# Performance work log

Hardware: AMD Instinct MI355X
Metric: run time of the kernel (lower is better)

## Reference

```python
import jax, jax.numpy as jnp
import numpy as np
import math

NUM_HEADS = 2


def setup_inputs() -> dict:
    key = jax.random.key(0)
    k1, k2, k3, k4 = jax.random.split(key, 4)
    B, S, E = 16, 2048, 8  # embed_dim == n_wires == 8 (required by module structure)
    x = jax.random.normal(k1, (B, S, E), dtype=jnp.float32)
    theta = jax.random.normal(k2, (E,), dtype=jnp.float32)          # trainable RX angles, one per wire
    w_out = jax.random.normal(k3, (E, E), dtype=jnp.float32) / math.sqrt(E)  # out_proj weight
    b_out = jax.random.normal(k4, (E,), dtype=jnp.float32) * 0.01   # out_proj bias
    return {"x": x, "theta": theta, "w_out": w_out, "b_out": b_out}


def reference(x, theta, w_out, b_out):
    B, S, E = x.shape
    H = NUM_HEADS
    dk = E // H
    # Quantum projection, analytic form: per-wire RX(x) then RX(theta) on |0>,
    # PauliZ expectation -> cos(x + theta). Same layer applied for q, k, v.
    q = jnp.cos(x + theta)              # [B, S, E]
    qh = q.reshape(B, S, H, dk).transpose(0, 2, 1, 3)  # [B, H, S, dk]; q == k == v
    scores = jnp.einsum('bhqd,bhkd->bhqk', qh, qh) / jnp.sqrt(jnp.float32(dk))
    attn = jax.nn.softmax(scores, axis=-1)             # dropout is identity in eval
    out = jnp.einsum('bhqk,bhkd->bhqd', attn, qh)      # [B, H, S, dk]
    out = out.transpose(0, 2, 1, 3).reshape(B, S, E)
    return out @ w_out.T + b_out
```

## Files before the change

kernel.cpp:

```cpp
#include <hip/hip_runtime.h>
#include <math.h>

#define BB 16
#define SS 2048
#define EE 8
#define HH 2
#define ROWS 128
#define TILES (SS / ROWS)
#define NCHUNK 4
#define CHUNK (SS / NCHUNK)
#define THREADS 512

typedef float vf2 __attribute__((ext_vector_type(2)));

#if defined(__has_builtin)
#if __has_builtin(__builtin_elementwise_fma)
#define HAS_EW_FMA 1
#endif
#endif

__device__ __forceinline__ float fast_exp2(float x) {
#if defined(__has_builtin)
#if __has_builtin(__builtin_amdgcn_exp2f)
  return __builtin_amdgcn_exp2f(x);
#else
  return exp2f(x);
#endif
#else
  return exp2f(x);
#endif
}

__device__ __forceinline__ vf2 pk_fma(vf2 a, vf2 b, vf2 c) {
#ifdef HAS_EW_FMA
  return __builtin_elementwise_fma(a, b, c);
#else
  vf2 r; r.x = fmaf(a.x, b.x, c.x); r.y = fmaf(a.y, b.y, c.y); return r;
#endif
}

__global__ __launch_bounds__(THREADS, 4)
void qattn_kernel(const float* __restrict__ x,
                  const float* __restrict__ theta,
                  const float* __restrict__ w_out,
                  const float* __restrict__ b_out,
                  float* __restrict__ out) {
  __shared__ float4 kv[HH * SS];

  const int b    = blockIdx.x >> 4;
  const int tile = blockIdx.x & 15;
  const int t    = threadIdx.x;

  const float4 th0 = ((const float4*)theta)[0];
  const float4 th1 = ((const float4*)theta)[1];

  const float4* x4 = (const float4*)x + (size_t)b * (SS * 2);
  for (int idx = t; idx < SS * 2; idx += THREADS) {
    const int s  = idx >> 1;
    const int hf = idx & 1;
    float4 xr = x4[idx];
    float4 th = hf ? th1 : th0;
    float4 kvv;
    kvv.x = cosf(xr.x + th.x);
    kvv.y = cosf(xr.y + th.y);
    kvv.z = cosf(xr.z + th.z);
    kvv.w = cosf(xr.w + th.w);
    kv[hf * SS + s] = kvv;
  }
  __syncthreads();

  const int lane = t & 63;
  const int w    = t >> 6;
  const int h    = w & 1;
  const int jc   = w >> 1;
  const int r0   = tile * ROWS + lane;
  const int r1   = r0 + 64;

  const float K_SCALE = 0.72134752044448170367f;
  float4 q0 = kv[h * SS + r0];
  float4 q1 = kv[h * SS + r1];
  vf2 q0xy = {q0.x * K_SCALE, q0.y * K_SCALE};
  vf2 q0zw = {q0.z * K_SCALE, q0.w * K_SCALE};
  vf2 q1xy = {q1.x * K_SCALE, q1.y * K_SCALE};
  vf2 q1zw = {q1.z * K_SCALE, q1.w * K_SCALE};

  float l0 = 0.f, l1 = 0.f;
  vf2 a0xy = {0.f, 0.f}, a0zw = {0.f, 0.f};
  vf2 a1xy = {0.f, 0.f}, a1zw = {0.f, 0.f};
  const float4* kp = &kv[h * SS + jc * CHUNK];
#pragma unroll 4
  for (int j = 0; j < CHUNK; ++j) {
    float4 k4 = kp[j];
    vf2 kxy = {k4.x, k4.y};
    vf2 kzw = {k4.z, k4.w};
    vf2 d0 = pk_fma(q0zw, kzw, q0xy * kxy);
    float p0 = fast_exp2(d0.x + d0.y);
    l0 += p0;
    vf2 pp0 = {p0, p0};
    a0xy = pk_fma(pp0, kxy, a0xy);
    a0zw = pk_fma(pp0, kzw, a0zw);
    vf2 d1 = pk_fma(q1zw, kzw, q1xy * kxy);
    float p1 = fast_exp2(d1.x + d1.y);
    l1 += p1;
    vf2 pp1 = {p1, p1};
    a1xy = pk_fma(pp1, kxy, a1xy);
    a1zw = pk_fma(pp1, kzw, a1zw);
  }

  __syncthreads();
  float* part = (float*)kv;
  float* ex   = (float*)kv + 5120;
  {
    float* p5 = part + (((jc * HH + h) * ROWS + lane) * 5);
    p5[0] = a0xy.x; p5[1] = a0xy.y; p5[2] = a0zw.x; p5[3] = a0zw.y; p5[4] = l0;
    p5 += 64 * 5;
    p5[0] = a1xy.x; p5[1] = a1xy.y; p5[2] = a1zw.x; p5[3] = a1zw.y; p5[4] = l1;
  }
  __syncthreads();

  if (t < ROWS * HH) {
    const int rr = t >> 1;
    const int hh = t & 1;
    float s0 = 0.f, s1 = 0.f, s2 = 0.f, s3 = 0.f, sl = 0.f;
#pragma unroll
    for (int jcc = 0; jcc < NCHUNK; ++jcc) {
      const float* p5 = part + (((jcc * HH + hh) * ROWS + rr) * 5);
      s0 += p5[0]; s1 += p5[1]; s2 += p5[2]; s3 += p5[3]; sl += p5[4];
    }
    const float inv = 1.0f / sl;
    ex[rr * 8 + hh * 4 + 0] = s0 * inv;
    ex[rr * 8 + hh * 4 + 1] = s1 * inv;
    ex[rr * 8 + hh * 4 + 2] = s2 * inv;
    ex[rr * 8 + hh * 4 + 3] = s3 * inv;
  }
  __syncthreads();

  if (t < ROWS * 2) {
    const int rr = t >> 1;
    const int hf = t & 1;
    const int e0 = hf * 4;
    float o[8];
#pragma unroll
    for (int j2 = 0; j2 < 8; ++j2) o[j2] = ex[rr * 8 + j2];
    float c0 = b_out[e0 + 0];
    float c1 = b_out[e0 + 1];
    float c2 = b_out[e0 + 2];
    float c3 = b_out[e0 + 3];
#pragma unroll
    for (int j2 = 0; j2 < 8; ++j2) {
      const float ov = o[j2];
      c0 = fmaf(ov, w_out[(e0 + 0) * 8 + j2], c0);
      c1 = fmaf(ov, w_out[(e0 + 1) * 8 + j2], c1);
      c2 = fmaf(ov, w_out[(e0 + 2) * 8 + j2], c2);
      c3 = fmaf(ov, w_out[(e0 + 3) * 8 + j2], c3);
    }
    const int grow = b * SS + tile * ROWS + rr;
    ((float4*)out)[grow * 2 + hf] = make_float4(c0, c1, c2, c3);
  }
}

extern "C" void kernel_launch(void* const* d_in, const int* in_sizes, int n_in,
                              void* d_out, int out_size, void* d_ws, size_t ws_size,
                              hipStream_t stream) {
  const float* x     = (const float*)d_in[0];
  const float* theta = (const float*)d_in[1];
  const float* w_out = (const float*)d_in[2];
  const float* b_out = (const float*)d_in[3];
  float* out = (float*)d_out;
  (void)in_sizes; (void)n_in; (void)out_size; (void)d_ws; (void)ws_size;

  dim3 grid(BB * TILES);
  qattn_kernel<<<dim3(BB * TILES), THREADS, 0, stream>>>(x, theta, w_out, b_out, out);
}
```

Baseline: 99.03 us.

## Split heads across blocks and combine output projection with atomics

Each block now handles a single head, so the grid doubles to 512 blocks. Each block uses 1024 threads and splits the keys into 16 chunks, and the shared-memory reduction is simpler. The output projection is split per head and summed into the output with atomicAdd, which needs a memset before the launch. Fast __cosf replaces cosf. The trade-offs are some loss of accuracy from __cosf, atomic contention, and an extra memset kernel.

```diff
diff --git a/kernel.cpp b/kernel.cpp
--- a/kernel.cpp
+++ b/kernel.cpp
@@ -3,13 +3,12 @@
 
 #define BB 16
 #define SS 2048
-#define EE 8
 #define HH 2
 #define ROWS 128
 #define TILES (SS / ROWS)
-#define NCHUNK 4
+#define NCHUNK 16
 #define CHUNK (SS / NCHUNK)
-#define THREADS 512
+#define THREADS 1024
 
 typedef float vf2 __attribute__((ext_vector_type(2)));
 
@@ -39,46 +38,42 @@
 #endif
 }
 
-__global__ __launch_bounds__(THREADS, 4)
+__global__ __launch_bounds__(THREADS, 8)
 void qattn_kernel(const float* __restrict__ x,
                   const float* __restrict__ theta,
                   const float* __restrict__ w_out,
                   const float* __restrict__ b_out,
                   float* __restrict__ out) {
-  __shared__ float4 kv[HH * SS];
+  __shared__ float4 sm4[SS + SS / 4];
+  float* lm = (float*)(sm4 + SS);
 
-  const int b    = blockIdx.x >> 4;
-  const int tile = blockIdx.x & 15;
+  const int bid  = blockIdx.x;
+  const int b    = bid >> 5;
+  const int tile = (bid >> 1) & 15;
+  const int h    = bid & 1;
   const int t    = threadIdx.x;
 
-  const float4 th0 = ((const float4*)theta)[0];
-  const float4 th1 = ((const float4*)theta)[1];
-
-  const float4* x4 = (const float4*)x + (size_t)b * (SS * 2);
-  for (int idx = t; idx < SS * 2; idx += THREADS) {
-    const int s  = idx >> 1;
-    const int hf = idx & 1;
-    float4 xr = x4[idx];
-    float4 th = hf ? th1 : th0;
+  const float4 th = ((const float4*)theta)[h];
+  const float4* x4 = (const float4*)x + (size_t)b * (SS * 2) + h;
+  for (int s = t; s < SS; s += THREADS) {
+    float4 xr = x4[2 * s];
     float4 kvv;
-    kvv.x = cosf(xr.x + th.x);
-    kvv.y = cosf(xr.y + th.y);
-    kvv.z = cosf(xr.z + th.z);
-    kvv.w = cosf(xr.w + th.w);
-    kv[hf * SS + s] = kvv;
+    kvv.x = __cosf(xr.x + th.x);
+    kvv.y = __cosf(xr.y + th.y);
+    kvv.z = __cosf(xr.z + th.z);
+    kvv.w = __cosf(xr.w + th.w);
+    sm4[s] = kvv;
   }
   __syncthreads();
 
   const int lane = t & 63;
-  const int w    = t >> 6;
-  const int h    = w & 1;
-  const int jc   = w >> 1;
+  const int jc   = t >> 6;
   const int r0   = tile * ROWS + lane;
   const int r1   = r0 + 64;
 
   const float K_SCALE = 0.72134752044448170367f;
-  float4 q0 = kv[h * SS + r0];
-  float4 q1 = kv[h * SS + r1];
+  float4 q0 = sm4[r0];
+  float4 q1 = sm4[r1];
   vf2 q0xy = {q0.x * K_SCALE, q0.y * K_SCALE};
   vf2 q0zw = {q0.z * K_SCALE, q0.w * K_SCALE};
   vf2 q1xy = {q1.x * K_SCALE, q1.y * K_SCALE};
@@ -87,20 +82,20 @@
   float l0 = 0.f, l1 = 0.f;
   vf2 a0xy = {0.f, 0.f}, a0zw = {0.f, 0.f};
   vf2 a1xy = {0.f, 0.f}, a1zw = {0.f, 0.f};
-  const float4* kp = &kv[h * SS + jc * CHUNK];
-#pragma unroll 4
+  const float4* kp = sm4 + jc * CHUNK;
+#pragma unroll 8
   for (int j = 0; j < CHUNK; ++j) {
     float4 k4 = kp[j];
     vf2 kxy = {k4.x, k4.y};
     vf2 kzw = {k4.z, k4.w};
     vf2 d0 = pk_fma(q0zw, kzw, q0xy * kxy);
     float p0 = fast_exp2(d0.x + d0.y);
+    vf2 d1 = pk_fma(q1zw, kzw, q1xy * kxy);
+    float p1 = fast_exp2(d1.x + d1.y);
     l0 += p0;
     vf2 pp0 = {p0, p0};
     a0xy = pk_fma(pp0, kxy, a0xy);
     a0zw = pk_fma(pp0, kzw, a0zw);
-    vf2 d1 = pk_fma(q1zw, kzw, q1xy * kxy);
-    float p1 = fast_exp2(d1.x + d1.y);
     l1 += p1;
     vf2 pp1 = {p1, p1};
     a1xy = pk_fma(pp1, kxy, a1xy);
@@ -108,54 +103,33 @@
   }
 
   __syncthreads();
-  float* part = (float*)kv;
-  float* ex   = (float*)kv + 5120;
   {
-    float* p5 = part + (((jc * HH + h) * ROWS + lane) * 5);
-    p5[0] = a0xy.x; p5[1] = a0xy.y; p5[2] = a0zw.x; p5[3] = a0zw.y; p5[4] = l0;
-    p5 += 64 * 5;
-    p5[0] = a1xy.x; p5[1] = a1xy.y; p5[2] = a1zw.x; p5[3] = a1zw.y; p5[4] = l1;
+    float4 v0 = make_float4(a0xy.x, a0xy.y, a0zw.x, a0zw.y);
+    float4 v1 = make_float4(a1xy.x, a1xy.y, a1zw.x, a1zw.y);
+    sm4[jc * ROWS + lane]      = v0;
+    sm4[jc * ROWS + lane + 64] = v1;
+    lm[jc * ROWS + lane]       = l0;
+    lm[jc * ROWS + lane + 64]  = l1;
   }
   __syncthreads();
 
-  if (t < ROWS * HH) {
-    const int rr = t >> 1;
-    const int hh = t & 1;
-    float s0 = 0.f, s1 = 0.f, s2 = 0.f, s3 = 0.f, sl = 0.f;
+  {
+    const int rr = t >> 3;
+    const int e  = t & 7;
+    float sx = 0.f, sy = 0.f, sz = 0.f, sw = 0.f, sl = 0.f;
 #pragma unroll
     for (int jcc = 0; jcc < NCHUNK; ++jcc) {
-      const float* p5 = part + (((jcc * HH + hh) * ROWS + rr) * 5);
-      s0 += p5[0]; s1 += p5[1]; s2 += p5[2]; s3 += p5[3]; sl += p5[4];
+      float4 a = sm4[jcc * ROWS + rr];
+      sx += a.x; sy += a.y; sz += a.z; sw += a.w;
+      sl += lm[jcc * ROWS + rr];
     }
     const float inv = 1.0f / sl;
-    ex[rr * 8 + hh * 4 + 0] = s0 * inv;
-    ex[rr * 8 + hh * 4 + 1] = s1 * inv;
-    ex[rr * 8 + hh * 4 + 2] = s2 * inv;
-    ex[rr * 8 + hh * 4 + 3] = s3 * inv;
-  }
-  __syncthreads();
-
-  if (t < ROWS * 2) {
-    const int rr = t >> 1;
-    const int hf = t & 1;
-    const int e0 = hf * 4;
-    float o[8];
-#pragma unroll
-    for (int j2 = 0; j2 < 8; ++j2) o[j2] = ex[rr * 8 + j2];
-    float c0 = b_out[e0 + 0];
-    float c1 = b_out[e0 + 1];
-    float c2 = b_out[e0 + 2];
-    float c3 = b_out[e0 + 3];
-#pragma unroll
-    for (int j2 = 0; j2 < 8; ++j2) {
-      const float ov = o[j2];
-      c0 = fmaf(ov, w_out[(e0 + 0) * 8 + j2], c0);
-      c1 = fmaf(ov, w_out[(e0 + 1) * 8 + j2], c1);
-      c2 = fmaf(ov, w_out[(e0 + 2) * 8 + j2], c2);
-      c3 = fmaf(ov, w_out[(e0 + 3) * 8 + j2], c3);
-    }
-    const int grow = b * SS + tile * ROWS + rr;
-    ((float4*)out)[grow * 2 + hf] = make_float4(c0, c1, c2, c3);
+    const float* wr = w_out + e * 8 + h * 4;
+    float val = fmaf(sx * inv, wr[0],
+                fmaf(sy * inv, wr[1],
+                fmaf(sz * inv, wr[2], (sw * inv) * wr[3])));
+    if (h == 0) val += b_out[e];
+    atomicAdd(out + ((size_t)(b * SS + tile * ROWS + rr)) * 8 + e, val);
   }
 }
 
@@ -167,8 +141,8 @@
   const float* w_out = (const float*)d_in[2];
   const float* b_out = (const float*)d_in[3];
   float* out = (float*)d_out;
-  (void)in_sizes; (void)n_in; (void)out_size; (void)d_ws; (void)ws_size;
+  (void)in_sizes; (void)n_in; (void)d_ws; (void)ws_size;
 
-  dim3 grid(BB * TILES);
-  qattn_kernel<<<dim3(BB * TILES), THREADS, 0, stream>>>(x, theta, w_out, b_out, out);
+  hipMemsetAsync(d_out, 0, (size_t)out_size * sizeof(float), stream);
+  qattn_kernel<<<dim3(BB * TILES * HH), THREADS, 0, stream>>>(x, theta, w_out, b_out, out);
 }
```

New measurement: 94.23 us. 4.8% less time.
